# Kernel tuning notes

Hardware: AMD Instinct MI355X
Metric: run time of the kernel (lower is better)

Reference implementation:

```python
import jax, jax.numpy as jnp
import numpy as np

B, T, C = 2, 4096, 512
H = 8
D = C // H  # head_dim = 64


def setup_inputs() -> dict:
    key = jax.random.key(0)
    ks = jax.random.split(key, 9)
    s = 0.02
    return {
        "x": jax.random.normal(ks[0], (B, T, C), dtype=jnp.float32),
        "wq": jax.random.normal(ks[1], (C, C), dtype=jnp.float32) * s,
        "bq": jnp.zeros((C,), dtype=jnp.float32),
        "wk": jax.random.normal(ks[2], (C, C), dtype=jnp.float32) * s,
        "bk": jnp.zeros((C,), dtype=jnp.float32),
        "wv": jax.random.normal(ks[3], (C, C), dtype=jnp.float32) * s,
        "bv": jnp.zeros((C,), dtype=jnp.float32),
        "wo": jax.random.normal(ks[4], (C, C), dtype=jnp.float32) * s,
        "bo": jnp.zeros((C,), dtype=jnp.float32),
    }


def reference(x, wq, bq, wk, bk, wv, bv, wo, bo):
    Bx, Tx, Cx = x.shape
    # projections: y = x @ W^T + b (torch Linear convention: W is [out, in])
    q = (x @ wq.T + bq).reshape(Bx, Tx, H, D).transpose(0, 2, 1, 3)  # [B,H,T,D]
    k = (x @ wk.T + bk).reshape(Bx, Tx, H, D).transpose(0, 2, 1, 3)
    v = (x @ wv.T + bv).reshape(Bx, Tx, H, D).transpose(0, 2, 1, 3)
    scores = jnp.einsum("bhqd,bhkd->bhqk", q, k) * (D ** -0.5)  # [B,H,T,T]
    causal = jnp.tril(jnp.ones((Tx, Tx), dtype=bool))
    scores = jnp.where(causal, scores, -jnp.inf)
    weights = jax.nn.softmax(scores, axis=-1)
    o = jnp.einsum("bhqk,bhkd->bhqd", weights, v)  # [B,H,T,D]
    o = o.transpose(0, 2, 1, 3).reshape(Bx, Tx, Cx)
    return o @ wo.T + bo
```

## Files before the change

### kernel.cpp

```cpp
#include <hip/hip_runtime.h>
#include <math.h>

static constexpr int Bb = 2;
static constexpr int Tt = 4096;
static constexpr int Cc = 512;
static constexpr int Hh = 8;
static constexpr int Dd = 64;
static constexpr int Mtot = Bb * Tt;

#define QSCALE 0.1803368801111f
#define DEFER_THR 11.5f

typedef __attribute__((ext_vector_type(8)))  short   short8;
typedef __attribute__((ext_vector_type(4)))  float   f32x4;
typedef __attribute__((ext_vector_type(16))) float   f32x16;
typedef __attribute__((ext_vector_type(4)))  unsigned int   uint4v;
typedef __attribute__((ext_vector_type(4)))  unsigned short ushort4v;

__device__ inline unsigned short f2bf(float f) {
    unsigned int u = __float_as_uint(f);
    u += 0x7fffu + ((u >> 16) & 1u);
    return (unsigned short)(u >> 16);
}

__device__ inline unsigned int cvtpk_bf16(float a, float b) {
    unsigned int r;
    asm("v_cvt_pk_bf16_f32 %0, %1, %2" : "=v"(r) : "v"(a), "v"(b));
    return r;
}

__device__ inline int SW(int row) { return (row ^ (row >> 3)) & 7; }

__device__ inline void gload16(const void* g, void* lds) {
    __builtin_amdgcn_global_load_lds(
        (const __attribute__((address_space(1))) void*)g,
        (__attribute__((address_space(3))) void*)lds, 16, 0, 0);
}

__global__ __launch_bounds__(256)
void cast_f32_bf16(const float* __restrict__ src, unsigned short* __restrict__ dst) {
    const size_t i = ((size_t)blockIdx.x * 256 + threadIdx.x) * 8;
    const float4 a = *reinterpret_cast<const float4*>(src + i);
    const float4 b = *reinterpret_cast<const float4*>(src + i + 4);
    short8 o;
    o[0] = (short)f2bf(a.x); o[1] = (short)f2bf(a.y);
    o[2] = (short)f2bf(a.z); o[3] = (short)f2bf(a.w);
    o[4] = (short)f2bf(b.x); o[5] = (short)f2bf(b.y);
    o[6] = (short)f2bf(b.z); o[7] = (short)f2bf(b.w);
    *reinterpret_cast<short8*>(dst + i) = o;
}

__global__ __launch_bounds__(256)
void cast_w4(const float* __restrict__ w0, const float* __restrict__ w1,
             const float* __restrict__ w2, const float* __restrict__ w3,
             unsigned short* __restrict__ dst) {
    const float* srcs[4] = {w0, w1, w2, w3};
    const float* s = srcs[blockIdx.y];
    unsigned short* d = dst + (size_t)blockIdx.y * (Cc * Cc);
    const size_t i = ((size_t)blockIdx.x * 256 + threadIdx.x) * 8;
    const float4 a = *reinterpret_cast<const float4*>(s + i);
    const float4 b = *reinterpret_cast<const float4*>(s + i + 4);
    short8 o;
    o[0] = (short)f2bf(a.x); o[1] = (short)f2bf(a.y);
    o[2] = (short)f2bf(a.z); o[3] = (short)f2bf(a.w);
    o[4] = (short)f2bf(b.x); o[5] = (short)f2bf(b.y);
    o[6] = (short)f2bf(b.z); o[7] = (short)f2bf(b.w);
    *reinterpret_cast<short8*>(d + i) = o;
}

__global__ __launch_bounds__(256)
void proj_qkv(const unsigned short* __restrict__ A, const unsigned short* __restrict__ Wall,
              const float* __restrict__ bq, const float* __restrict__ bk,
              const float* __restrict__ bv,
              unsigned short* __restrict__ qo, unsigned short* __restrict__ ko,
              unsigned short* __restrict__ vo) {
    __shared__ unsigned short As[128][32];
    __shared__ unsigned short Bs[128][32];

    const int which = blockIdx.z;
    const unsigned short* Wb = Wall + (size_t)which * Cc * Cc;
    const float* bias = (which == 0) ? bq : (which == 1) ? bk : bv;
    unsigned short* outp = (which == 0) ? qo : (which == 1) ? ko : vo;
    const float scale = (which == 0) ? QSCALE : 1.0f;

    const int tid = threadIdx.x;
    const int lane = tid & 63;
    const int w = tid >> 6;
    const int wr = w >> 1, wc = w & 1;
    const int l15 = lane & 15, lg = lane >> 4;
    const int m0 = blockIdx.x * 128, n0 = blockIdx.y * 128;

    f32x4 acc[4][4] = {};

    for (int k0 = 0; k0 < Cc; k0 += 32) {
        #pragma unroll
        for (int i = 0; i < 2; ++i) {
            const int idx = tid + i * 256;
            const int row = idx >> 2, g = idx & 3;
            *reinterpret_cast<short8*>(&As[row][g * 8]) =
                *reinterpret_cast<const short8*>(&A[(size_t)(m0 + row) * Cc + k0 + g * 8]);
            *reinterpret_cast<short8*>(&Bs[row][g * 8]) =
                *reinterpret_cast<const short8*>(&Wb[(size_t)(n0 + row) * Cc + k0 + g * 8]);
        }
        __syncthreads();
        short8 a[4], b[4];
        #pragma unroll
        for (int mi = 0; mi < 4; ++mi)
            a[mi] = *reinterpret_cast<const short8*>(&As[wr * 64 + mi * 16 + l15][lg * 8]);
        #pragma unroll
        for (int nj = 0; nj < 4; ++nj)
            b[nj] = *reinterpret_cast<const short8*>(&Bs[wc * 64 + nj * 16 + l15][lg * 8]);
        #pragma unroll
        for (int mi = 0; mi < 4; ++mi)
            #pragma unroll
            for (int nj = 0; nj < 4; ++nj)
                acc[mi][nj] = __builtin_amdgcn_mfma_f32_16x16x32_bf16(a[mi], b[nj], acc[mi][nj], 0, 0, 0);
        __syncthreads();
    }

    #pragma unroll
    for (int mi = 0; mi < 4; ++mi) {
        #pragma unroll
        for (int nj = 0; nj < 4; ++nj) {
            const int col = n0 + wc * 64 + nj * 16 + l15;
            const float bvv = bias[col];
            if (which == 2) {
                const int mbase = m0 + wr * 64 + mi * 16 + lg * 4;
                const int b_ = mbase >> 12, t = mbase & (Tt - 1);
                const int h = col >> 6, d = col & 63;
                ushort4v o;
                #pragma unroll
                for (int r = 0; r < 4; ++r)
                    o[r] = f2bf(acc[mi][nj][r] + bvv);
                *reinterpret_cast<ushort4v*>(
                    &outp[(((size_t)b_ * Hh + h) * Dd + d) * Tt + t]) = o;
            } else {
                #pragma unroll
                for (int r = 0; r < 4; ++r) {
                    const int row = m0 + wr * 64 + mi * 16 + lg * 4 + r;
                    const int b_ = row >> 12, t = row & (Tt - 1);
                    const int h = col >> 6, d = col & 63;
                    outp[(((size_t)b_ * Hh + h) * Tt + t) * Dd + d] =
                        f2bf((acc[mi][nj][r] + bvv) * scale);
                }
            }
        }
    }
}

__global__ __launch_bounds__(256)
void proj_out(const unsigned short* __restrict__ A, const unsigned short* __restrict__ Wb,
              const float* __restrict__ bias, float* __restrict__ outp) {
    __shared__ unsigned short As[128][32];
    __shared__ unsigned short Bs[128][32];

    const int tid = threadIdx.x;
    const int lane = tid & 63;
    const int w = tid >> 6;
    const int wr = w >> 1, wc = w & 1;
    const int l15 = lane & 15, lg = lane >> 4;
    const int m0 = blockIdx.x * 128, n0 = blockIdx.y * 128;

    f32x4 acc[4][4] = {};

    for (int k0 = 0; k0 < Cc; k0 += 32) {
        #pragma unroll
        for (int i = 0; i < 2; ++i) {
            const int idx = tid + i * 256;
            const int row = idx >> 2, g = idx & 3;
            *reinterpret_cast<short8*>(&As[row][g * 8]) =
                *reinterpret_cast<const short8*>(&A[(size_t)(m0 + row) * Cc + k0 + g * 8]);
            *reinterpret_cast<short8*>(&Bs[row][g * 8]) =
                *reinterpret_cast<const short8*>(&Wb[(size_t)(n0 + row) * Cc + k0 + g * 8]);
        }
        __syncthreads();
        short8 a[4], b[4];
        #pragma unroll
        for (int mi = 0; mi < 4; ++mi)
            a[mi] = *reinterpret_cast<const short8*>(&As[wr * 64 + mi * 16 + l15][lg * 8]);
        #pragma unroll
        for (int nj = 0; nj < 4; ++nj)
            b[nj] = *reinterpret_cast<const short8*>(&Bs[wc * 64 + nj * 16 + l15][lg * 8]);
        #pragma unroll
        for (int mi = 0; mi < 4; ++mi)
            #pragma unroll
            for (int nj = 0; nj < 4; ++nj)
                acc[mi][nj] = __builtin_amdgcn_mfma_f32_16x16x32_bf16(a[mi], b[nj], acc[mi][nj], 0, 0, 0);
        __syncthreads();
    }

    #pragma unroll
    for (int mi = 0; mi < 4; ++mi) {
        #pragma unroll
        for (int nj = 0; nj < 4; ++nj) {
            const int col = n0 + wc * 64 + nj * 16 + l15;
            const float bv = bias[col];
            #pragma unroll
            for (int r = 0; r < 4; ++r) {
                const int row = m0 + wr * 64 + mi * 16 + lg * 4 + r;
                outp[(size_t)row * Cc + col] = acc[mi][nj][r] + bv;
            }
        }
    }
}

__global__ __launch_bounds__(256)
void attn_mfma(const unsigned short* __restrict__ qb, const unsigned short* __restrict__ kb,
               const unsigned short* __restrict__ vtb,
               float* __restrict__ opart, float2* __restrict__ mlp) {
    __shared__ unsigned short Ks[2][64][64];
    __shared__ unsigned short Vts[2][64][64];
    __shared__ float stats[4][32];

    const int bid = (int)blockIdx.x;
    const int half = bid >> 9;
    const int idx = bid & 511;
    const int qt = half ? (idx >> 4) : (31 - (idx >> 4));
    const int s  = half;
    const int bh = idx & 15;
    const int t0 = s ? (qt + 1) : 0;
    const int t1 = s ? (2 * qt + 2) : (qt + 1);

    const int tid = threadIdx.x;
    const int w = tid >> 6;
    const int lane = tid & 63;
    const int l31 = lane & 31, hi = lane >> 5;

    const int qg = qt * 128 + w * 32 + l31;

    short8 qf[4];
    {
        const unsigned short* qp = qb + ((size_t)bh * Tt + qg) * Dd + hi * 8;
        #pragma unroll
        for (int sl = 0; sl < 4; ++sl)
            qf[sl] = *reinterpret_cast<const short8*>(qp + sl * 16);
    }

    const unsigned short* kb_h = kb + (size_t)bh * Tt * Dd;
    const unsigned short* vt_h = vtb + (size_t)bh * Dd * Tt;
    const int r0 = (w << 4) + (lane >> 3);
    const int r1 = r0 + 8;
    const int gk0 = ((lane & 7) ^ SW(r0)) * 8;
    const int gk1 = ((lane & 7) ^ SW(r1)) * 8;

    auto STAGE = [&](int t) {
        const int n64 = t * 64;
        const int bufi = t & 1;
        gload16(kb_h + (size_t)(n64 + r0) * Dd + gk0, &Ks[bufi][(w << 4)][0]);
        gload16(kb_h + (size_t)(n64 + r1) * Dd + gk1, &Ks[bufi][(w << 4) + 8][0]);
        gload16(vt_h + (size_t)r0 * Tt + n64 + gk0, &Vts[bufi][(w << 4)][0]);
        gload16(vt_h + (size_t)r1 * Tt + n64 + gk1, &Vts[bufi][(w << 4) + 8][0]);
    };

    f32x16 oacc[2] = {};
    float mrow = -INFINITY, lrow = 0.f;

    const int qmax_w = qt * 128 + w * 32 + 31;
    const int qmin_w = qt * 128 + w * 32;

    STAGE(t0);

    for (int kt = t0; kt < t1; ++kt) {
        const int cur = kt & 1;
        asm volatile("s_waitcnt vmcnt(0)" ::: "memory");
        __builtin_amdgcn_s_barrier();
        __builtin_amdgcn_sched_barrier(0);

        if (kt + 1 < t1) STAGE(kt + 1);

        if (kt * 64 <= qmax_w) {
            f32x16 sacc[2];
            #pragma unroll
            for (int f = 0; f < 2; ++f) {
                f32x16 z = {};
                const int krow = f * 32 + l31;
                const int sw = SW(krow);
                #pragma unroll
                for (int sl = 0; sl < 4; ++sl) {
                    const short8 kf = *reinterpret_cast<const short8*>(
                        &Ks[cur][krow][((2 * sl + hi) ^ sw) * 8]);
                    z = __builtin_amdgcn_mfma_f32_32x32x16_bf16(kf, qf[sl], z, 0, 0, 0);
                }
                sacc[f] = z;
            }

            if (kt * 64 + 63 > qmin_w) {
                #pragma unroll
                for (int f = 0; f < 2; ++f)
                    #pragma unroll
                    for (int r = 0; r < 16; ++r) {
                        const int kvg = kt * 64 + f * 32 + (r & 3) + 8 * (r >> 2) + 4 * hi;
                        if (kvg > qg) sacc[f][r] = -INFINITY;
                    }
            }

            float tr[16];
            #pragma unroll
            for (int r = 0; r < 16; ++r) tr[r] = fmaxf(sacc[0][r], sacc[1][r]);
            #pragma unroll
            for (int st = 8; st >= 1; st >>= 1)
                #pragma unroll
                for (int r = 0; r < 8; ++r)
                    if (r < st) tr[r] = fmaxf(tr[r], tr[r + st]);
            float pmax = fmaxf(tr[0], __shfl_xor(tr[0], 32));

            if (__any(pmax > mrow + DEFER_THR)) {
                const float mnew = fmaxf(mrow, pmax);
                const float corr = exp2f(mrow - mnew);
                mrow = mnew;
                lrow *= corr;
                stats[w][l31] = corr;
                #pragma unroll
                for (int r = 0; r < 16; ++r) {
                    const float c = stats[w][(r & 3) + 8 * (r >> 2) + 4 * hi];
                    oacc[0][r] *= c;
                    oacc[1][r] *= c;
                }
            }

            float rs = 0.f;
            #pragma unroll
            for (int f = 0; f < 2; ++f)
                #pragma unroll
                for (int r = 0; r < 16; ++r) {
                    const float p = exp2f(sacc[f][r] - mrow);
                    sacc[f][r] = p;
                    rs += p;
                }
            lrow += rs;

            #pragma unroll
            for (int f = 0; f < 2; ++f) {
                #pragma unroll
                for (int s2 = 0; s2 < 2; ++s2) {
                    const int b0 = s2 * 8;
                    unsigned int c01 = cvtpk_bf16(sacc[f][b0 + 0], sacc[f][b0 + 1]);
                    unsigned int c23 = cvtpk_bf16(sacc[f][b0 + 2], sacc[f][b0 + 3]);
                    unsigned int c45 = cvtpk_bf16(sacc[f][b0 + 4], sacc[f][b0 + 5]);
                    unsigned int c67 = cvtpk_bf16(sacc[f][b0 + 6], sacc[f][b0 + 7]);
                    asm("v_permlane32_swap_b32 %0, %1" : "+v"(c01), "+v"(c45));
                    asm("v_permlane32_swap_b32 %0, %1" : "+v"(c23), "+v"(c67));
                    uint4v paw;
                    paw[0] = c01; paw[1] = c23; paw[2] = c45; paw[3] = c67;
                    const short8 pa = *reinterpret_cast<short8*>(&paw);
                    const int g = 4 * f + 2 * s2;
                    #pragma unroll
                    for (int nb = 0; nb < 2; ++nb) {
                        const int vrow = nb * 32 + l31;
                        const short8 vf = *reinterpret_cast<const short8*>(
                            &Vts[cur][vrow][((g + hi) ^ SW(vrow)) * 8]);
                        oacc[nb] = __builtin_amdgcn_mfma_f32_32x32x16_bf16(pa, vf, oacc[nb], 0, 0, 0);
                    }
                }
            }
        }
    }

    const float lf = lrow + __shfl_xor(lrow, 32);
    const size_t pbase = ((size_t)s * 16 + bh) * Tt;
    if (hi == 0) mlp[pbase + qg] = make_float2(mrow, lf);
    #pragma unroll
    for (int r = 0; r < 16; ++r) {
        const int qr = (r & 3) + 8 * (r >> 2) + 4 * hi;
        const int tg = qt * 128 + w * 32 + qr;
        float* dst = opart + (pbase + tg) * 64 + l31;
        dst[0]  = oacc[0][r];
        dst[32] = oacc[1][r];
    }
}

__global__ __launch_bounds__(256)
void combine(const float* __restrict__ opart, const float2* __restrict__ mlp,
             unsigned short* __restrict__ ob) {
    const int tid = threadIdx.x;
    const int row = (int)blockIdx.x * 16 + (tid >> 4);
    const int c4 = (tid & 15) * 4;
    const size_t halfRows = (size_t)16 * Tt;

    const float2 ml0 = mlp[row];
    const float2 ml1 = mlp[halfRows + row];
    const float m = fmaxf(ml0.x, ml1.x);
    const float s0 = exp2f(ml0.x - m), s1 = exp2f(ml1.x - m);
    const float inv = 1.f / (ml0.y * s0 + ml1.y * s1);

    const float4 o0 = *reinterpret_cast<const float4*>(&opart[(size_t)row * 64 + c4]);
    const float4 o1 = *reinterpret_cast<const float4*>(&opart[(halfRows + row) * 64 + c4]);

    ushort4v o;
    o[0] = f2bf((o0.x * s0 + o1.x * s1) * inv);
    o[1] = f2bf((o0.y * s0 + o1.y * s1) * inv);
    o[2] = f2bf((o0.z * s0 + o1.z * s1) * inv);
    o[3] = f2bf((o0.w * s0 + o1.w * s1) * inv);

    const int bh = row >> 12, t = row & (Tt - 1);
    const int b_ = bh >> 3, h = bh & 7;
    *reinterpret_cast<ushort4v*>(&ob[((size_t)b_ * Tt + t) * Cc + h * Dd + c4]) = o;
}

extern "C" void kernel_launch(void* const* d_in, const int* in_sizes, int n_in,
                              void* d_out, int out_size, void* d_ws, size_t ws_size,
                              hipStream_t stream) {
    const float* x  = (const float*)d_in[0];
    const float* wq = (const float*)d_in[1];
    const float* bq = (const float*)d_in[2];
    const float* wk = (const float*)d_in[3];
    const float* bk = (const float*)d_in[4];
    const float* wv = (const float*)d_in[5];
    const float* bv = (const float*)d_in[6];
    const float* wo = (const float*)d_in[7];
    const float* bo = (const float*)d_in[8];
    float* out = (float*)d_out;

    const size_t nTok = (size_t)Mtot * Cc;
    const size_t nW   = (size_t)Cc * Cc;

    unsigned short* xb    = (unsigned short*)d_ws;
    unsigned short* wqb   = xb + nTok;
    unsigned short* wob   = wqb + 3 * nW;
    unsigned short* qbuf  = wqb + 4 * nW;
    unsigned short* kbuf  = qbuf + nTok;
    unsigned short* vtbuf = kbuf + nTok;
    unsigned short* oattb = vtbuf + nTok;
    float*  opart = (float*)(oattb + nTok);
    float2* mlp   = (float2*)(opart + (size_t)2 * 16 * Tt * 64);

    cast_f32_bf16<<<dim3((unsigned)(nTok / 8 / 256)), 256, 0, stream>>>(x, xb);
    cast_w4<<<dim3((unsigned)(nW / 8 / 256), 4), 256, 0, stream>>>(wq, wk, wv, wo, wqb);

    proj_qkv<<<dim3(Mtot / 128, Cc / 128, 3), 256, 0, stream>>>(
        xb, wqb, bq, bk, bv, qbuf, kbuf, vtbuf);

    attn_mfma<<<dim3(1024), 256, 0, stream>>>(qbuf, kbuf, vtbuf, opart, mlp);

    combine<<<dim3(16 * Tt / 16), 256, 0, stream>>>(opart, mlp, oattb);

    proj_out<<<dim3(Mtot / 128, Cc / 128), 256, 0, stream>>>(oattb, wob, bo, out);
}
```

Measured before the change: 170.0 us.

## Use persistent atomic work queue with 4-way KV split and bf16 partials

Result: faster. 162.4 us (-4.4%).

```diff
diff --git a/kernel.cpp b/kernel.cpp
--- a/kernel.cpp
+++ b/kernel.cpp
@@ -10,6 +10,7 @@
 
 #define QSCALE 0.1803368801111f
 #define DEFER_THR 11.5f
+#define NTICK 2048
 
 typedef __attribute__((ext_vector_type(8)))  short   short8;
 typedef __attribute__((ext_vector_type(4)))  float   f32x4;
@@ -22,6 +23,9 @@
     u += 0x7fffu + ((u >> 16) & 1u);
     return (unsigned short)(u >> 16);
 }
+__device__ inline float bf2f(unsigned short u) {
+    return __uint_as_float((unsigned int)u << 16);
+}
 
 __device__ inline unsigned int cvtpk_bf16(float a, float b) {
     unsigned int r;
@@ -38,7 +42,9 @@
 }
 
 __global__ __launch_bounds__(256)
-void cast_f32_bf16(const float* __restrict__ src, unsigned short* __restrict__ dst) {
+void cast_f32_bf16(const float* __restrict__ src, unsigned short* __restrict__ dst,
+                   int* __restrict__ ctr) {
+    if (blockIdx.x == 0 && threadIdx.x == 0) *ctr = 0;
     const size_t i = ((size_t)blockIdx.x * 256 + threadIdx.x) * 8;
     const float4 a = *reinterpret_cast<const float4*>(src + i);
     const float4 b = *reinterpret_cast<const float4*>(src + i + 4);
@@ -207,190 +213,213 @@
 __global__ __launch_bounds__(256)
 void attn_mfma(const unsigned short* __restrict__ qb, const unsigned short* __restrict__ kb,
                const unsigned short* __restrict__ vtb,
-               float* __restrict__ opart, float2* __restrict__ mlp) {
+               unsigned short* __restrict__ opart, float2* __restrict__ mlp,
+               int* __restrict__ ctr) {
     __shared__ unsigned short Ks[2][64][64];
     __shared__ unsigned short Vts[2][64][64];
     __shared__ float stats[4][32];
-
-    const int bid = (int)blockIdx.x;
-    const int half = bid >> 9;
-    const int idx = bid & 511;
-    const int qt = half ? (idx >> 4) : (31 - (idx >> 4));
-    const int s  = half;
-    const int bh = idx & 15;
-    const int t0 = s ? (qt + 1) : 0;
-    const int t1 = s ? (2 * qt + 2) : (qt + 1);
+    __shared__ int tkt;
 
     const int tid = threadIdx.x;
     const int w = tid >> 6;
     const int lane = tid & 63;
     const int l31 = lane & 31, hi = lane >> 5;
 
-    const int qg = qt * 128 + w * 32 + l31;
-
-    short8 qf[4];
-    {
-        const unsigned short* qp = qb + ((size_t)bh * Tt + qg) * Dd + hi * 8;
-        #pragma unroll
-        for (int sl = 0; sl < 4; ++sl)
-            qf[sl] = *reinterpret_cast<const short8*>(qp + sl * 16);
-    }
-
-    const unsigned short* kb_h = kb + (size_t)bh * Tt * Dd;
-    const unsigned short* vt_h = vtb + (size_t)bh * Dd * Tt;
     const int r0 = (w << 4) + (lane >> 3);
     const int r1 = r0 + 8;
     const int gk0 = ((lane & 7) ^ SW(r0)) * 8;
     const int gk1 = ((lane & 7) ^ SW(r1)) * 8;
 
-    auto STAGE = [&](int t) {
-        const int n64 = t * 64;
-        const int bufi = t & 1;
-        gload16(kb_h + (size_t)(n64 + r0) * Dd + gk0, &Ks[bufi][(w << 4)][0]);
-        gload16(kb_h + (size_t)(n64 + r1) * Dd + gk1, &Ks[bufi][(w << 4) + 8][0]);
-        gload16(vt_h + (size_t)r0 * Tt + n64 + gk0, &Vts[bufi][(w << 4)][0]);
-        gload16(vt_h + (size_t)r1 * Tt + n64 + gk1, &Vts[bufi][(w << 4) + 8][0]);
-    };
-
-    f32x16 oacc[2] = {};
-    float mrow = -INFINITY, lrow = 0.f;
-
-    const int qmax_w = qt * 128 + w * 32 + 31;
-    const int qmin_w = qt * 128 + w * 32;
-
-    STAGE(t0);
-
-    for (int kt = t0; kt < t1; ++kt) {
-        const int cur = kt & 1;
-        asm volatile("s_waitcnt vmcnt(0)" ::: "memory");
-        __builtin_amdgcn_s_barrier();
-        __builtin_amdgcn_sched_barrier(0);
-
-        if (kt + 1 < t1) STAGE(kt + 1);
-
-        if (kt * 64 <= qmax_w) {
-            f32x16 sacc[2];
+    for (;;) {
+        __syncthreads();
+        if (tid == 0) tkt = atomicAdd(ctr, 1);
+        __syncthreads();
+        const int t = tkt;
+        if (t >= NTICK) break;
+
+        const int qt = 31 - (t >> 6);
+        const int ch = (t >> 4) & 3;
+        const int bh = t & 15;
+        const int n  = 2 * qt + 2;
+        const int t0 = (n * ch) >> 2;
+        const int t1 = (n * (ch + 1)) >> 2;
+
+        const int qg = qt * 128 + w * 32 + l31;
+
+        short8 qf[4];
+        {
+            const unsigned short* qp = qb + ((size_t)bh * Tt + qg) * Dd + hi * 8;
             #pragma unroll
-            for (int f = 0; f < 2; ++f) {
-                f32x16 z = {};
-                const int krow = f * 32 + l31;
-                const int sw = SW(krow);
-                #pragma unroll
-                for (int sl = 0; sl < 4; ++sl) {
-                    const short8 kf = *reinterpret_cast<const short8*>(
-                        &Ks[cur][krow][((2 * sl + hi) ^ sw) * 8]);
-                    z = __builtin_amdgcn_mfma_f32_32x32x16_bf16(kf, qf[sl], z, 0, 0, 0);
+            for (int sl = 0; sl < 4; ++sl)
+                qf[sl] = *reinterpret_cast<const short8*>(qp + sl * 16);
+        }
+
+        const unsigned short* kb_h = kb + (size_t)bh * Tt * Dd;
+        const unsigned short* vt_h = vtb + (size_t)bh * Dd * Tt;
+
+        f32x16 oacc[2] = {};
+        float mrow = -INFINITY, lrow = 0.f;
+
+        const int qmax_w = qt * 128 + w * 32 + 31;
+        const int qmin_w = qt * 128 + w * 32;
+
+        if (t0 < t1) {
+            {
+                const int n64 = t0 * 64, bufi = t0 & 1;
+                gload16(kb_h + (size_t)(n64 + r0) * Dd + gk0, &Ks[bufi][(w << 4)][0]);
+                gload16(kb_h + (size_t)(n64 + r1) * Dd + gk1, &Ks[bufi][(w << 4) + 8][0]);
+                gload16(vt_h + (size_t)r0 * Tt + n64 + gk0, &Vts[bufi][(w << 4)][0]);
+                gload16(vt_h + (size_t)r1 * Tt + n64 + gk1, &Vts[bufi][(w << 4) + 8][0]);
+            }
+
+            for (int kt = t0; kt < t1; ++kt) {
+                const int cur = kt & 1;
+                asm volatile("s_waitcnt vmcnt(0)" ::: "memory");
+                __builtin_amdgcn_s_barrier();
+                __builtin_amdgcn_sched_barrier(0);
+
+                if (kt + 1 < t1) {
+                    const int n64 = (kt + 1) * 64, bufi = (kt + 1) & 1;
+                    gload16(kb_h + (size_t)(n64 + r0) * Dd + gk0, &Ks[bufi][(w << 4)][0]);
+                    gload16(kb_h + (size_t)(n64 + r1) * Dd + gk1, &Ks[bufi][(w << 4) + 8][0]);
+                    gload16(vt_h + (size_t)r0 * Tt + n64 + gk0, &Vts[bufi][(w << 4)][0]);
+                    gload16(vt_h + (size_t)r1 * Tt + n64 + gk1, &Vts[bufi][(w << 4) + 8][0]);
                 }
-                sacc[f] = z;
-            }
-
-            if (kt * 64 + 63 > qmin_w) {
-                #pragma unroll
-                for (int f = 0; f < 2; ++f)
+
+                if (kt * 64 <= qmax_w) {
+                    f32x16 sacc[2];
+                    __builtin_amdgcn_s_setprio(1);
                     #pragma unroll
-                    for (int r = 0; r < 16; ++r) {
-                        const int kvg = kt * 64 + f * 32 + (r & 3) + 8 * (r >> 2) + 4 * hi;
-                        if (kvg > qg) sacc[f][r] = -INFINITY;
+                    for (int f = 0; f < 2; ++f) {
+                        f32x16 z = {};
+                        const int krow = f * 32 + l31;
+                        const int sw = SW(krow);
+                        #pragma unroll
+                        for (int sl = 0; sl < 4; ++sl) {
+                            const short8 kf = *reinterpret_cast<const short8*>(
+                                &Ks[cur][krow][((2 * sl + hi) ^ sw) * 8]);
+                            z = __builtin_amdgcn_mfma_f32_32x32x16_bf16(kf, qf[sl], z, 0, 0, 0);
+                        }
+                        sacc[f] = z;
                     }
-            }
-
-            float tr[16];
-            #pragma unroll
-            for (int r = 0; r < 16; ++r) tr[r] = fmaxf(sacc[0][r], sacc[1][r]);
-            #pragma unroll
-            for (int st = 8; st >= 1; st >>= 1)
-                #pragma unroll
-                for (int r = 0; r < 8; ++r)
-                    if (r < st) tr[r] = fmaxf(tr[r], tr[r + st]);
-            float pmax = fmaxf(tr[0], __shfl_xor(tr[0], 32));
-
-            if (__any(pmax > mrow + DEFER_THR)) {
-                const float mnew = fmaxf(mrow, pmax);
-                const float corr = exp2f(mrow - mnew);
-                mrow = mnew;
-                lrow *= corr;
-                stats[w][l31] = corr;
-                #pragma unroll
-                for (int r = 0; r < 16; ++r) {
-                    const float c = stats[w][(r & 3) + 8 * (r >> 2) + 4 * hi];
-                    oacc[0][r] *= c;
-                    oacc[1][r] *= c;
-                }
-            }
-
-            float rs = 0.f;
-            #pragma unroll
-            for (int f = 0; f < 2; ++f)
-                #pragma unroll
-                for (int r = 0; r < 16; ++r) {
-                    const float p = exp2f(sacc[f][r] - mrow);
-                    sacc[f][r] = p;
-                    rs += p;
-                }
-            lrow += rs;
-
-            #pragma unroll
-            for (int f = 0; f < 2; ++f) {
-                #pragma unroll
-                for (int s2 = 0; s2 < 2; ++s2) {
-                    const int b0 = s2 * 8;
-                    unsigned int c01 = cvtpk_bf16(sacc[f][b0 + 0], sacc[f][b0 + 1]);
-                    unsigned int c23 = cvtpk_bf16(sacc[f][b0 + 2], sacc[f][b0 + 3]);
-                    unsigned int c45 = cvtpk_bf16(sacc[f][b0 + 4], sacc[f][b0 + 5]);
-                    unsigned int c67 = cvtpk_bf16(sacc[f][b0 + 6], sacc[f][b0 + 7]);
-                    asm("v_permlane32_swap_b32 %0, %1" : "+v"(c01), "+v"(c45));
-                    asm("v_permlane32_swap_b32 %0, %1" : "+v"(c23), "+v"(c67));
-                    uint4v paw;
-                    paw[0] = c01; paw[1] = c23; paw[2] = c45; paw[3] = c67;
-                    const short8 pa = *reinterpret_cast<short8*>(&paw);
-                    const int g = 4 * f + 2 * s2;
+                    __builtin_amdgcn_s_setprio(0);
+
+                    if (kt * 64 + 63 > qmin_w) {
+                        #pragma unroll
+                        for (int f = 0; f < 2; ++f)
+                            #pragma unroll
+                            for (int r = 0; r < 16; ++r) {
+                                const int kvg = kt * 64 + f * 32 + (r & 3) + 8 * (r >> 2) + 4 * hi;
+                                if (kvg > qg) sacc[f][r] = -INFINITY;
+                            }
+                    }
+
+                    float tr[16];
                     #pragma unroll
-                    for (int nb = 0; nb < 2; ++nb) {
-                        const int vrow = nb * 32 + l31;
-                        const short8 vf = *reinterpret_cast<const short8*>(
-                            &Vts[cur][vrow][((g + hi) ^ SW(vrow)) * 8]);
-                        oacc[nb] = __builtin_amdgcn_mfma_f32_32x32x16_bf16(pa, vf, oacc[nb], 0, 0, 0);
+                    for (int r = 0; r < 16; ++r) tr[r] = fmaxf(sacc[0][r], sacc[1][r]);
+                    #pragma unroll
+                    for (int st = 8; st >= 1; st >>= 1)
+                        #pragma unroll
+                        for (int r = 0; r < 8; ++r)
+                            if (r < st) tr[r] = fmaxf(tr[r], tr[r + st]);
+                    float pmax = fmaxf(tr[0], __shfl_xor(tr[0], 32));
+
+                    if (__any(pmax > mrow + DEFER_THR)) {
+                        const float mnew = fmaxf(mrow, pmax);
+                        const float corr = exp2f(mrow - mnew);
+                        mrow = mnew;
+                        lrow *= corr;
+                        stats[w][l31] = corr;
+                        #pragma unroll
+                        for (int r = 0; r < 16; ++r) {
+                            const float c = stats[w][(r & 3) + 8 * (r >> 2) + 4 * hi];
+                            oacc[0][r] *= c;
+                            oacc[1][r] *= c;
+                        }
+                    }
+
+                    float rs = 0.f;
+                    #pragma unroll
+                    for (int f = 0; f < 2; ++f)
+                        #pragma unroll
+                        for (int r = 0; r < 16; ++r) {
+                            const float p = exp2f(sacc[f][r] - mrow);
+                            sacc[f][r] = p;
+                            rs += p;
+                        }
+                    lrow += rs;
+
+                    #pragma unroll
+                    for (int f = 0; f < 2; ++f) {
+                        #pragma unroll
+                        for (int s2 = 0; s2 < 2; ++s2) {
+                            const int b0 = s2 * 8;
+                            unsigned int c01 = cvtpk_bf16(sacc[f][b0 + 0], sacc[f][b0 + 1]);
+                            unsigned int c23 = cvtpk_bf16(sacc[f][b0 + 2], sacc[f][b0 + 3]);
+                            unsigned int c45 = cvtpk_bf16(sacc[f][b0 + 4], sacc[f][b0 + 5]);
+                            unsigned int c67 = cvtpk_bf16(sacc[f][b0 + 6], sacc[f][b0 + 7]);
+                            asm("v_permlane32_swap_b32 %0, %1" : "+v"(c01), "+v"(c45));
+                            asm("v_permlane32_swap_b32 %0, %1" : "+v"(c23), "+v"(c67));
+                            uint4v paw;
+                            paw[0] = c01; paw[1] = c23; paw[2] = c45; paw[3] = c67;
+                            const short8 pa = *reinterpret_cast<short8*>(&paw);
+                            const int g = 4 * f + 2 * s2;
+                            __builtin_amdgcn_s_setprio(1);
+                            #pragma unroll
+                            for (int nb = 0; nb < 2; ++nb) {
+                                const int vrow = nb * 32 + l31;
+                                const short8 vf = *reinterpret_cast<const short8*>(
+                                    &Vts[cur][vrow][((g + hi) ^ SW(vrow)) * 8]);
+                                oacc[nb] = __builtin_amdgcn_mfma_f32_32x32x16_bf16(pa, vf, oacc[nb], 0, 0, 0);
+                            }
+                            __builtin_amdgcn_s_setprio(0);
+                        }
                     }
                 }
             }
         }
+
+        const float lf = lrow + __shfl_xor(lrow, 32);
+        const size_t pbase = ((size_t)ch * 16 + bh) * Tt;
+        if (hi == 0) mlp[pbase + qg] = make_float2(mrow, lf);
+        #pragma unroll
+        for (int r = 0; r < 16; ++r) {
+            const int qr = (r & 3) + 8 * (r >> 2) + 4 * hi;
+            const int tg = qt * 128 + w * 32 + qr;
+            unsigned short* dst = opart + (pbase + tg) * 64 + l31;
+            dst[0]  = f2bf(oacc[0][r]);
+            dst[32] = f2bf(oacc[1][r]);
+        }
     }
-
-    const float lf = lrow + __shfl_xor(lrow, 32);
-    const size_t pbase = ((size_t)s * 16 + bh) * Tt;
-    if (hi == 0) mlp[pbase + qg] = make_float2(mrow, lf);
-    #pragma unroll
-    for (int r = 0; r < 16; ++r) {
-        const int qr = (r & 3) + 8 * (r >> 2) + 4 * hi;
-        const int tg = qt * 128 + w * 32 + qr;
-        float* dst = opart + (pbase + tg) * 64 + l31;
-        dst[0]  = oacc[0][r];
-        dst[32] = oacc[1][r];
-    }
-}
-
-__global__ __launch_bounds__(256)
-void combine(const float* __restrict__ opart, const float2* __restrict__ mlp,
+}
+
+__global__ __launch_bounds__(256)
+void combine(const unsigned short* __restrict__ opart, const float2* __restrict__ mlp,
              unsigned short* __restrict__ ob) {
     const int tid = threadIdx.x;
     const int row = (int)blockIdx.x * 16 + (tid >> 4);
     const int c4 = (tid & 15) * 4;
-    const size_t halfRows = (size_t)16 * Tt;
+    const size_t cs = (size_t)16 * Tt;
 
     const float2 ml0 = mlp[row];
-    const float2 ml1 = mlp[halfRows + row];
-    const float m = fmaxf(ml0.x, ml1.x);
+    const float2 ml1 = mlp[cs + row];
+    const float2 ml2 = mlp[2 * cs + row];
+    const float2 ml3 = mlp[3 * cs + row];
+    const float m = fmaxf(fmaxf(ml0.x, ml1.x), fmaxf(ml2.x, ml3.x));
     const float s0 = exp2f(ml0.x - m), s1 = exp2f(ml1.x - m);
-    const float inv = 1.f / (ml0.y * s0 + ml1.y * s1);
-
-    const float4 o0 = *reinterpret_cast<const float4*>(&opart[(size_t)row * 64 + c4]);
-    const float4 o1 = *reinterpret_cast<const float4*>(&opart[(halfRows + row) * 64 + c4]);
+    const float s2 = exp2f(ml2.x - m), s3 = exp2f(ml3.x - m);
+    const float inv = 1.f / (ml0.y * s0 + ml1.y * s1 + ml2.y * s2 + ml3.y * s3);
+
+    const ushort4v p0 = *reinterpret_cast<const ushort4v*>(&opart[(0 * cs + row) * 64 + c4]);
+    const ushort4v p1 = *reinterpret_cast<const ushort4v*>(&opart[(1 * cs + row) * 64 + c4]);
+    const ushort4v p2 = *reinterpret_cast<const ushort4v*>(&opart[(2 * cs + row) * 64 + c4]);
+    const ushort4v p3 = *reinterpret_cast<const ushort4v*>(&opart[(3 * cs + row) * 64 + c4]);
 
     ushort4v o;
-    o[0] = f2bf((o0.x * s0 + o1.x * s1) * inv);
-    o[1] = f2bf((o0.y * s0 + o1.y * s1) * inv);
-    o[2] = f2bf((o0.z * s0 + o1.z * s1) * inv);
-    o[3] = f2bf((o0.w * s0 + o1.w * s1) * inv);
+    #pragma unroll
+    for (int e = 0; e < 4; ++e)
+        o[e] = f2bf((bf2f(p0[e]) * s0 + bf2f(p1[e]) * s1 +
+                     bf2f(p2[e]) * s2 + bf2f(p3[e]) * s3) * inv);
 
     const int bh = row >> 12, t = row & (Tt - 1);
     const int b_ = bh >> 3, h = bh & 7;
@@ -421,16 +450,17 @@
     unsigned short* kbuf  = qbuf + nTok;
     unsigned short* vtbuf = kbuf + nTok;
     unsigned short* oattb = vtbuf + nTok;
-    float*  opart = (float*)(oattb + nTok);
-    float2* mlp   = (float2*)(opart + (size_t)2 * 16 * Tt * 64);
-
-    cast_f32_bf16<<<dim3((unsigned)(nTok / 8 / 256)), 256, 0, stream>>>(x, xb);
+    unsigned short* opart = oattb + nTok;
+    float2* mlp = (float2*)(opart + (size_t)4 * 16 * Tt * 64);
+    int*    ctr = (int*)(mlp + (size_t)4 * 16 * Tt);
+
+    cast_f32_bf16<<<dim3((unsigned)(nTok / 8 / 256)), 256, 0, stream>>>(x, xb, ctr);
     cast_w4<<<dim3((unsigned)(nW / 8 / 256), 4), 256, 0, stream>>>(wq, wk, wv, wo, wqb);
 
     proj_qkv<<<dim3(Mtot / 128, Cc / 128, 3), 256, 0, stream>>>(
         xb, wqb, bq, bk, bv, qbuf, kbuf, vtbuf);
 
-    attn_mfma<<<dim3(1024), 256, 0, stream>>>(qbuf, kbuf, vtbuf, opart, mlp);
+    attn_mfma<<<dim3(1024), 256, 0, stream>>>(qbuf, kbuf, vtbuf, opart, mlp, ctr);
 
     combine<<<dim3(16 * Tt / 16), 256, 0, stream>>>(opart, mlp, oattb);
 
```
